# Kernel tuning notes

Measured on AMD Instinct MI355X. Metric: run time of the kernel, lower is better.

Reference implementation:

```python
import jax, jax.numpy as jnp
import numpy as np

B, L, H = 512, 1000, 128  # batch, time steps, hidden size


def setup_inputs() -> dict:
    key = jax.random.key(0)
    ks = jax.random.split(key, 12)
    s = 1.0 / np.sqrt(H)

    def u(k, shape):
        return jax.random.uniform(k, shape, jnp.float32, -s, s)

    return {
        "y": jax.random.normal(ks[0], (B, L), jnp.float32),
        # LSTMCell 1: input size 1 -> H (torch gate order i, f, g, o)
        "W_ih1": u(ks[1], (4 * H, 1)),
        "W_hh1": u(ks[2], (4 * H, H)),
        "b_ih1": u(ks[3], (4 * H,)),
        "b_hh1": u(ks[4], (4 * H,)),
        # LSTMCell 2: H -> H
        "W_ih2": u(ks[5], (4 * H, H)),
        "W_hh2": u(ks[6], (4 * H, H)),
        "b_ih2": u(ks[7], (4 * H,)),
        "b_hh2": u(ks[8], (4 * H,)),
        # Linear H -> 1
        "W_lin": u(ks[9], (1, H)),
        "b_lin": u(ks[10], (1,)),
    }


def _lstm_cell(x, h, c, W_ih, W_hh, b_ih, b_hh):
    # torch.nn.LSTMCell: gates = x W_ih^T + b_ih + h W_hh^T + b_hh, order i,f,g,o
    g = x @ W_ih.T + b_ih + h @ W_hh.T + b_hh  # [B, 4H]
    i, f, gg, o = jnp.split(g, 4, axis=-1)
    i = jax.nn.sigmoid(i)
    f = jax.nn.sigmoid(f)
    gg = jnp.tanh(gg)
    o = jax.nn.sigmoid(o)
    c_new = f * c + i * gg
    h_new = o * jnp.tanh(c_new)
    return h_new, c_new


def reference(y, W_ih1, W_hh1, b_ih1, b_hh1, W_ih2, W_hh2, b_ih2, b_hh2, W_lin, b_lin):
    n = y.shape[0]
    z = jnp.zeros((n, H), y.dtype)

    def step(carry, x_t):
        h1, c1, h2, c2 = carry
        x_t = x_t[:, None]  # [B, 1]
        h1, c1 = _lstm_cell(x_t, h1, c1, W_ih1, W_hh1, b_ih1, b_hh1)
        h2, c2 = _lstm_cell(h1, h2, c2, W_ih2, W_hh2, b_ih2, b_hh2)
        out = h2 @ W_lin.T + b_lin  # [B, 1]
        return (h1, c1, h2, c2), out[:, 0]

    _, outs = jax.lax.scan(step, (z, z, z, z), y.T)  # outs: [L, B]
    return outs.T  # [B, L]
```

## Files before the change

### kernel.cpp

```cpp
#include <hip/hip_runtime.h>

typedef _Float16 half2_t __attribute__((ext_vector_type(2)));
typedef _Float16 half8_t __attribute__((ext_vector_type(8)));

union h8pack { half8_t v; half2_t h2[4]; };

constexpr int BATCH = 512;
constexpr int SEQ   = 1000;
constexpr int HID   = 128;
constexpr int GATES = 4 * HID;
constexpr int TPB   = 512;
constexpr int ROWS  = 2;

#if __has_builtin(__builtin_amdgcn_fdot2)
__device__ __forceinline__ float fdot2(half2_t a, half2_t b, float c) {
  return __builtin_amdgcn_fdot2(a, b, c, false);
}
#else
__device__ __forceinline__ float fdot2(half2_t a, half2_t b, float c) {
  return c + (float)a[0] * (float)b[0] + (float)a[1] * (float)b[1];
}
#endif

__device__ __forceinline__ float fast_sigmoid(float x) {
  x = fminf(fmaxf(x, -30.f), 30.f);
  return __fdividef(1.f, 1.f + __expf(-x));
}
__device__ __forceinline__ float fast_tanh(float x) {
  x = fminf(fmaxf(x, -15.f), 15.f);
  float e = __expf(2.f * x);
  return __fdividef(e - 1.f, e + 1.f);
}

__global__ __launch_bounds__(TPB, 1)
void lstm_persist(const float* __restrict__ y,
                  const float* __restrict__ W_ih1,
                  const float* __restrict__ W_hh1,
                  const float* __restrict__ b_ih1,
                  const float* __restrict__ b_hh1,
                  const float* __restrict__ W_ih2,
                  const float* __restrict__ W_hh2,
                  const float* __restrict__ b_ih2,
                  const float* __restrict__ b_hh2,
                  const float* __restrict__ W_lin,
                  const float* __restrict__ b_lin,
                  float* __restrict__ out)
{
  const int tid = threadIdx.x;
  const int j   = tid;
  const int r0  = blockIdx.x * ROWS;

  __shared__ alignas(16) half8_t h1_sh[ROWS][HID / 8];
  __shared__ alignas(16) half8_t h2_sh[ROWS][HID / 8];
  __shared__ float g1_sh[ROWS][GATES];
  __shared__ float g2_sh[ROWS][GATES];
  __shared__ float red_sh[4];

  half2_t w1[HID / 2], w2[HID / 2], w3[HID / 2];
  {
    const float2* p1 = (const float2*)(W_hh1 + (size_t)j * HID);
    const float2* p2 = (const float2*)(W_ih2 + (size_t)j * HID);
    const float2* p3 = (const float2*)(W_hh2 + (size_t)j * HID);
#pragma unroll
    for (int k = 0; k < HID / 2; ++k) {
      float2 a  = p1[k]; w1[k] = half2_t{(_Float16)a.x,  (_Float16)a.y};
      float2 bb = p2[k]; w2[k] = half2_t{(_Float16)bb.x, (_Float16)bb.y};
      float2 cc = p3[k]; w3[k] = half2_t{(_Float16)cc.x, (_Float16)cc.y};
    }
  }
  const float wih1  = W_ih1[j];
  const float bias1 = b_ih1[j] + b_hh1[j];
  const float bias2 = b_ih2[j] + b_hh2[j];
  const float wlin  = W_lin[tid & (HID - 1)];
  const float blin  = b_lin[0];

  if (tid < 64) {
    half8_t z = {};
    if (tid < 32) ((half8_t*)h1_sh)[tid] = z;
    else          ((half8_t*)h2_sh)[tid - 32] = z;
  }
  __syncthreads();

  const float* xr0 = y + (size_t)r0 * SEQ;
  const float* xr1 = xr0 + SEQ;
  float c1v = 0.f, c2v = 0.f;

  float x0 = xr0[0], x1 = xr1[0];

  for (int t = 0; t < SEQ; ++t) {
    const int tn = (t + 1 < SEQ) ? (t + 1) : t;
    float nx0 = xr0[tn], nx1 = xr1[tn];

    float a0 = fmaf(x0, wih1, bias1);
    float a1 = fmaf(x1, wih1, bias1);
#pragma unroll
    for (int c = 0; c < HID / 8; ++c) {
      h8pack u0, u1;
      u0.v = h1_sh[0][c];
      u1.v = h1_sh[1][c];
#pragma unroll
      for (int q = 0; q < 4; ++q) {
        a0 = fdot2(w1[4 * c + q], u0.h2[q], a0);
        a1 = fdot2(w1[4 * c + q], u1.h2[q], a1);
      }
    }
    g1_sh[0][j] = a0;
    g1_sh[1][j] = a1;
    __syncthreads();

    if (tid < ROWS * HID) {
      const int r = tid >> 7, jj = tid & (HID - 1);
      float gi = g1_sh[r][jj];
      float gf = g1_sh[r][jj + HID];
      float gg = g1_sh[r][jj + 2 * HID];
      float go = g1_sh[r][jj + 3 * HID];
      float iv = fast_sigmoid(gi);
      float fv = fast_sigmoid(gf);
      float gv = fast_tanh(gg);
      float ov = fast_sigmoid(go);
      c1v = fmaf(fv, c1v, iv * gv);
      float h = ov * fast_tanh(c1v);
      ((_Float16*)h1_sh)[tid] = (_Float16)h;
    }
    __syncthreads();

    float s0a = bias2, s1a = bias2, s0b = 0.f, s1b = 0.f;
#pragma unroll
    for (int c = 0; c < HID / 8; ++c) {
      h8pack u0, u1, v0, v1;
      u0.v = h1_sh[0][c];
      u1.v = h1_sh[1][c];
      v0.v = h2_sh[0][c];
      v1.v = h2_sh[1][c];
#pragma unroll
      for (int q = 0; q < 4; ++q) {
        s0a = fdot2(w2[4 * c + q], u0.h2[q], s0a);
        s1a = fdot2(w2[4 * c + q], u1.h2[q], s1a);
        s0b = fdot2(w3[4 * c + q], v0.h2[q], s0b);
        s1b = fdot2(w3[4 * c + q], v1.h2[q], s1b);
      }
    }
    g2_sh[0][j] = s0a + s0b;
    g2_sh[1][j] = s1a + s1b;
    __syncthreads();

    float pred = 0.f;
    if (tid < ROWS * HID) {
      const int r = tid >> 7, jj = tid & (HID - 1);
      float gi = g2_sh[r][jj];
      float gf = g2_sh[r][jj + HID];
      float gg = g2_sh[r][jj + 2 * HID];
      float go = g2_sh[r][jj + 3 * HID];
      float iv = fast_sigmoid(gi);
      float fv = fast_sigmoid(gf);
      float gv = fast_tanh(gg);
      float ov = fast_sigmoid(go);
      c2v = fmaf(fv, c2v, iv * gv);
      float h = ov * fast_tanh(c2v);
      ((_Float16*)h2_sh)[tid] = (_Float16)h;
      pred = h * wlin;
#pragma unroll
      for (int off = 32; off > 0; off >>= 1)
        pred += __shfl_down(pred, off);
      if ((tid & 63) == 0) red_sh[tid >> 6] = pred;
    }
    __syncthreads();
    if (tid < ROWS) {
      out[(size_t)(r0 + tid) * SEQ + t] = red_sh[2 * tid] + red_sh[2 * tid + 1] + blin;
    }
    x0 = nx0;
    x1 = nx1;
  }
}

extern "C" void kernel_launch(void* const* d_in, const int* in_sizes, int n_in,
                              void* d_out, int out_size, void* d_ws, size_t ws_size,
                              hipStream_t stream) {
  const float* y     = (const float*)d_in[0];
  const float* W_ih1 = (const float*)d_in[1];
  const float* W_hh1 = (const float*)d_in[2];
  const float* b_ih1 = (const float*)d_in[3];
  const float* b_hh1 = (const float*)d_in[4];
  const float* W_ih2 = (const float*)d_in[5];
  const float* W_hh2 = (const float*)d_in[6];
  const float* b_ih2 = (const float*)d_in[7];
  const float* b_hh2 = (const float*)d_in[8];
  const float* W_lin = (const float*)d_in[9];
  const float* b_lin = (const float*)d_in[10];
  float* out = (float*)d_out;

  lstm_persist<<<BATCH / ROWS, TPB, 0, stream>>>(
      y, W_ih1, W_hh1, b_ih1, b_hh1, W_ih2, W_hh2, b_ih2, b_hh2, W_lin, b_lin, out);
}
```

Baseline: 3.014 ms.

## Park layer-2 weights in AGPRs and overlap W_hh2 dot with layer-1 phase

Layer-2 weights move from VGPRs into accumulation registers via inline v_accvgpr_write/read, and launch bounds allow two blocks per CU. The h2·W_hh2 product is computed during the layer-1 phase, since h2 from the previous step is already available there, leaving only h1·W_ih2 on the critical path after the layer-1 update. The aim is higher occupancy and a shorter dependent chain per step. The cost is an extra AGPR read per weight, more shared memory for the split partial sums, and a fragile asm dependence on the register allocator.

```diff
diff --git a/kernel.cpp b/kernel.cpp
--- a/kernel.cpp
+++ b/kernel.cpp
@@ -22,6 +22,16 @@
 }
 #endif
 
+__device__ __forceinline__ void awrite(float& dst, half2_t w) {
+  asm volatile("v_accvgpr_write_b32 %0, %1"
+               : "=a"(dst) : "v"(__builtin_bit_cast(float, w)));
+}
+__device__ __forceinline__ half2_t aread(const float& a) {
+  float f;
+  asm volatile("v_accvgpr_read_b32 %0, %1" : "=v"(f) : "a"(a));
+  return __builtin_bit_cast(half2_t, f);
+}
+
 __device__ __forceinline__ float fast_sigmoid(float x) {
   x = fminf(fmaxf(x, -30.f), 30.f);
   return __fdividef(1.f, 1.f + __expf(-x));
@@ -32,7 +42,7 @@
   return __fdividef(e - 1.f, e + 1.f);
 }
 
-__global__ __launch_bounds__(TPB, 1)
+__global__ __launch_bounds__(TPB, 2)
 void lstm_persist(const float* __restrict__ y,
                   const float* __restrict__ W_ih1,
                   const float* __restrict__ W_hh1,
@@ -53,21 +63,29 @@
   __shared__ alignas(16) half8_t h1_sh[ROWS][HID / 8];
   __shared__ alignas(16) half8_t h2_sh[ROWS][HID / 8];
   __shared__ float g1_sh[ROWS][GATES];
-  __shared__ float g2_sh[ROWS][GATES];
+  __shared__ float d2_sh[ROWS][GATES];
+  __shared__ float d3_sh[ROWS][GATES];
   __shared__ float red_sh[4];
 
-  half2_t w1[HID / 2], w2[HID / 2], w3[HID / 2];
+  half2_t w1[HID / 2];
   {
     const float2* p1 = (const float2*)(W_hh1 + (size_t)j * HID);
+#pragma unroll
+    for (int k = 0; k < HID / 2; ++k) {
+      float2 a = p1[k]; w1[k] = half2_t{(_Float16)a.x, (_Float16)a.y};
+    }
+  }
+  float aw2[HID / 2], aw3[HID / 2];
+  {
     const float2* p2 = (const float2*)(W_ih2 + (size_t)j * HID);
     const float2* p3 = (const float2*)(W_hh2 + (size_t)j * HID);
 #pragma unroll
     for (int k = 0; k < HID / 2; ++k) {
-      float2 a  = p1[k]; w1[k] = half2_t{(_Float16)a.x,  (_Float16)a.y};
-      float2 bb = p2[k]; w2[k] = half2_t{(_Float16)bb.x, (_Float16)bb.y};
-      float2 cc = p3[k]; w3[k] = half2_t{(_Float16)cc.x, (_Float16)cc.y};
-    }
-  }
+      float2 a = p2[k]; awrite(aw2[k], half2_t{(_Float16)a.x, (_Float16)a.y});
+      float2 b = p3[k]; awrite(aw3[k], half2_t{(_Float16)b.x, (_Float16)b.y});
+    }
+  }
+
   const float wih1  = W_ih1[j];
   const float bias1 = b_ih1[j] + b_hh1[j];
   const float bias2 = b_ih2[j] + b_hh2[j];
@@ -84,7 +102,6 @@
   const float* xr0 = y + (size_t)r0 * SEQ;
   const float* xr1 = xr0 + SEQ;
   float c1v = 0.f, c2v = 0.f;
-
   float x0 = xr0[0], x1 = xr1[0];
 
   for (int t = 0; t < SEQ; ++t) {
@@ -93,19 +110,27 @@
 
     float a0 = fmaf(x0, wih1, bias1);
     float a1 = fmaf(x1, wih1, bias1);
+    float s0 = bias2, s1 = bias2;
 #pragma unroll
     for (int c = 0; c < HID / 8; ++c) {
-      h8pack u0, u1;
+      h8pack u0, u1, v0, v1;
       u0.v = h1_sh[0][c];
       u1.v = h1_sh[1][c];
+      v0.v = h2_sh[0][c];
+      v1.v = h2_sh[1][c];
 #pragma unroll
       for (int q = 0; q < 4; ++q) {
         a0 = fdot2(w1[4 * c + q], u0.h2[q], a0);
         a1 = fdot2(w1[4 * c + q], u1.h2[q], a1);
+        half2_t w3v = aread(aw3[4 * c + q]);
+        s0 = fdot2(w3v, v0.h2[q], s0);
+        s1 = fdot2(w3v, v1.h2[q], s1);
       }
     }
     g1_sh[0][j] = a0;
     g1_sh[1][j] = a1;
+    d3_sh[0][j] = s0;
+    d3_sh[1][j] = s1;
     __syncthreads();
 
     if (tid < ROWS * HID) {
@@ -124,33 +149,30 @@
     }
     __syncthreads();
 
-    float s0a = bias2, s1a = bias2, s0b = 0.f, s1b = 0.f;
+    float p0 = 0.f, p1 = 0.f;
 #pragma unroll
     for (int c = 0; c < HID / 8; ++c) {
-      h8pack u0, u1, v0, v1;
+      h8pack u0, u1;
       u0.v = h1_sh[0][c];
       u1.v = h1_sh[1][c];
-      v0.v = h2_sh[0][c];
-      v1.v = h2_sh[1][c];
 #pragma unroll
       for (int q = 0; q < 4; ++q) {
-        s0a = fdot2(w2[4 * c + q], u0.h2[q], s0a);
-        s1a = fdot2(w2[4 * c + q], u1.h2[q], s1a);
-        s0b = fdot2(w3[4 * c + q], v0.h2[q], s0b);
-        s1b = fdot2(w3[4 * c + q], v1.h2[q], s1b);
+        half2_t w2v = aread(aw2[4 * c + q]);
+        p0 = fdot2(w2v, u0.h2[q], p0);
+        p1 = fdot2(w2v, u1.h2[q], p1);
       }
     }
-    g2_sh[0][j] = s0a + s0b;
-    g2_sh[1][j] = s1a + s1b;
+    d2_sh[0][j] = p0;
+    d2_sh[1][j] = p1;
     __syncthreads();
 
     float pred = 0.f;
     if (tid < ROWS * HID) {
       const int r = tid >> 7, jj = tid & (HID - 1);
-      float gi = g2_sh[r][jj];
-      float gf = g2_sh[r][jj + HID];
-      float gg = g2_sh[r][jj + 2 * HID];
-      float go = g2_sh[r][jj + 3 * HID];
+      float gi = d2_sh[r][jj]           + d3_sh[r][jj];
+      float gf = d2_sh[r][jj + HID]     + d3_sh[r][jj + HID];
+      float gg = d2_sh[r][jj + 2 * HID] + d3_sh[r][jj + 2 * HID];
+      float go = d2_sh[r][jj + 3 * HID] + d3_sh[r][jj + 3 * HID];
       float iv = fast_sigmoid(gi);
       float fv = fast_sigmoid(gf);
       float gv = fast_tanh(gg);
```

Measured after the change: 3.577 ms. 1.19x slower.
